# Kernel tuning notes

Measured on AMD Instinct MI355X. Metric: run time of the kernel, lower is better.

## Reference

```python
import jax, jax.numpy as jnp
import numpy as np

DIM = 512
HEADS = 8
DIM_HEAD = 64
INNER = HEADS * DIM_HEAD


def setup_inputs() -> dict:
    key = jax.random.key(0)
    k1, k2, k3, k4 = jax.random.split(key, 4)
    x = jax.random.normal(k1, (4, 8192, DIM), dtype=jnp.float32)
    # nn.Linear(dim, inner*3, bias=False): weight applied as x @ W^T; store transposed form [dim, 3*inner]
    w_qkv = jax.random.normal(k2, (DIM, 3 * INNER), dtype=jnp.float32) / np.sqrt(DIM)
    w_out = jax.random.normal(k3, (INNER, DIM), dtype=jnp.float32) / np.sqrt(INNER)
    b_out = jax.random.normal(k4, (DIM,), dtype=jnp.float32) * 0.01
    return {"x": x, "w_qkv": w_qkv, "w_out": w_out, "b_out": b_out}


def reference(x, w_qkv, w_out, b_out):
    b, n, d = x.shape
    qkv = x @ w_qkv  # [b, n, 3*inner]
    q, k, v = jnp.split(qkv, 3, axis=-1)

    def to_heads(t):
        return t.reshape(b, n, HEADS, DIM_HEAD).transpose(0, 2, 1, 3)  # [b,h,n,dh]

    q, k, v = map(to_heads, (q, k, v))
    q = jax.nn.elu(q) + 1.0
    k = jax.nn.elu(k) + 1.0
    # kv summary: [b,h,dh,dh]
    kv = jnp.einsum('bhnd,bhnm->bhdm', k, v)
    # normalizer z: [b,h,n]  (note: original does NOT apply self.scale)
    z = 1.0 / (jnp.einsum('bhnd,bhd->bhn', q, k.sum(axis=2)) + 1e-6)
    out = jnp.einsum('bhnd,bhdm->bhnm', q, kv) * z[..., None]  # [b,h,n,dh]
    out = out.transpose(0, 2, 1, 3).reshape(b, n, INNER)
    return out @ w_out + b_out
```

## Files before the change

kernel.cpp:

```cpp
#include <hip/hip_runtime.h>
#include <hip/hip_bf16.h>

#define B_SZ 4
#define SEQ 8192
#define DIM 512
#define HEADS 8
#define DH 64
#define INNER 512
#define QKV_COLS 1536
#define M_TOT (B_SZ * SEQ)
#define BHN (B_SZ * HEADS)

typedef __bf16 bf16x8 __attribute__((ext_vector_type(8)));
typedef __bf16 bf16x4 __attribute__((ext_vector_type(4)));
typedef float f32x4 __attribute__((ext_vector_type(4)));

__device__ __forceinline__ float elu1(float x) {
    return x > 0.f ? x + 1.f : __expf(x);
}

__device__ __forceinline__ void gl_lds16(const void* g, void* l) {
    __builtin_amdgcn_global_load_lds(
        (const __attribute__((address_space(1))) unsigned int*)g,
        (__attribute__((address_space(3))) unsigned int*)l, 16, 0, 0);
}

#define MFMA16(a, b, c) __builtin_amdgcn_mfma_f32_16x16x32_bf16(a, b, c, 0, 0, 0)
#define BARRIER() asm volatile("s_barrier" ::: "memory")

__global__ void convert_all(const float* __restrict__ x,
                            const float* __restrict__ w_qkv,
                            const float* __restrict__ w_out,
                            __bf16* __restrict__ xb,
                            __bf16* __restrict__ wqkv_t,
                            __bf16* __restrict__ wout_t) {
    const int NX = M_TOT * DIM / 4;
    int id = blockIdx.x * 256 + threadIdx.x;
    if (id < NX) {
        float4 f = reinterpret_cast<const float4*>(x)[id];
        bf16x4 h = {(__bf16)f.x, (__bf16)f.y, (__bf16)f.z, (__bf16)f.w};
        reinterpret_cast<bf16x4*>(xb)[id] = h;
        return;
    }
    int id2 = id - NX;
    if (id2 < QKV_COLS * DIM) {
        int n = id2 / DIM, k = id2 % DIM;
        wqkv_t[id2] = (__bf16)w_qkv[k * QKV_COLS + n];
    } else {
        int id3 = id2 - QKV_COLS * DIM;
        if (id3 < INNER * DIM) {
            int n = id3 / DIM, k = id3 % DIM;
            wout_t[id3] = (__bf16)w_out[k * DIM + n];
        }
    }
}

#define TSTR 136
__launch_bounds__(256, 2)
__global__ void gemm_qkv(const __bf16* __restrict__ xb,
                         const __bf16* __restrict__ wqkv_t,
                         __bf16* __restrict__ q_ws,
                         __bf16* __restrict__ kT_ws,
                         __bf16* __restrict__ vT_ws) {
    __shared__ __attribute__((aligned(16))) char smem[128 * TSTR * 2];
    __bf16* As = (__bf16*)smem;
    __bf16* Bs = (__bf16*)(smem + 16384);
    __bf16* T  = (__bf16*)smem;

    const int tid = threadIdx.x;
    const int wid = tid >> 6;
    const int lane = tid & 63;
    const int wm = wid >> 1, wn = wid & 1;
    const int lq = lane >> 4, lr = lane & 15;
    const int f  = blockIdx.y * gridDim.x + blockIdx.x;
    const int xc = f & 7, sl = f >> 3;
    const int ml = sl / 12, nn = sl % 12;
    const int m0 = (xc * 32 + ml) * 128;
    const int n0 = nn * 128;
    const int lrow = lane >> 3;
    const int lsw  = ((lane & 7) ^ lrow) * 8;

    f32x4 acc[4][4] = {};

    for (int kb = 0; kb < DIM; kb += 64) {
#pragma unroll
        for (int t = 0; t < 4; ++t) {
            int qi = wid * 4 + t;
            int row = qi * 8 + lrow;
            gl_lds16(&xb[(size_t)(m0 + row) * DIM + kb + lsw], &As[qi * 512]);
            gl_lds16(&wqkv_t[(size_t)(n0 + row) * DIM + kb + lsw], &Bs[qi * 512]);
        }
        __syncthreads();
#pragma unroll
        for (int ks = 0; ks < 2; ++ks) {
            const int csw = ((ks * 4 + lq) ^ (lr & 7)) * 8;
            bf16x8 af[4], bfv[4];
#pragma unroll
            for (int i = 0; i < 4; ++i)
                af[i] = *reinterpret_cast<const bf16x8*>(
                    &As[(wm * 64 + i * 16 + lr) * 64 + csw]);
#pragma unroll
            for (int j = 0; j < 4; ++j)
                bfv[j] = *reinterpret_cast<const bf16x8*>(
                    &Bs[(wn * 64 + j * 16 + lr) * 64 + csw]);
#pragma unroll
            for (int i = 0; i < 4; ++i)
#pragma unroll
                for (int j = 0; j < 4; ++j)
                    acc[i][j] = MFMA16(af[i], bfv[j], acc[i][j]);
        }
        __syncthreads();
    }

    const int which = n0 / INNER;
    const int n0w = n0 % INNER;
    const int b = m0 / SEQ;
    const int nbase = m0 % SEQ;

    if (which == 0) {
#pragma unroll
        for (int i = 0; i < 4; ++i)
#pragma unroll
            for (int j = 0; j < 4; ++j) {
                int col = wn * 64 + j * 16 + lr;
#pragma unroll
                for (int r = 0; r < 4; ++r)
                    T[(wm * 64 + i * 16 + lq * 4 + r) * TSTR + col] =
                        (__bf16)elu1(acc[i][j][r]);
            }
        __syncthreads();
#pragma unroll
        for (int it = 0; it < 8; ++it) {
            int c = tid + it * 256;
            int row = c >> 4, dc = (c & 15) * 8;
            bf16x8 v = *reinterpret_cast<const bf16x8*>(&T[row * TSTR + dc]);
            int col = n0w + dc;
            int h = col >> 6, d = col & 63;
            *reinterpret_cast<bf16x8*>(
                &q_ws[(((size_t)(b * HEADS + h)) * SEQ + nbase + row) * DH + d]) = v;
        }
    } else {
        __bf16* dst = (which == 1) ? kT_ws : vT_ws;
#pragma unroll
        for (int i = 0; i < 4; ++i)
#pragma unroll
            for (int j = 0; j < 4; ++j) {
                int col = wn * 64 + j * 16 + lr;
                int rowb = wm * 64 + i * 16 + lq * 4;
                bf16x4 h4;
#pragma unroll
                for (int r = 0; r < 4; ++r) {
                    float v = acc[i][j][r];
                    h4[r] = (__bf16)((which == 1) ? elu1(v) : v);
                }
                *reinterpret_cast<bf16x4*>(&T[col * TSTR + rowb]) = h4;
            }
        __syncthreads();
#pragma unroll
        for (int it = 0; it < 8; ++it) {
            int c = tid + it * 256;
            int colIdx = c >> 4, rc = (c & 15) * 8;
            bf16x8 v = *reinterpret_cast<const bf16x8*>(&T[colIdx * TSTR + rc]);
            int gcol = n0w + colIdx;
            int h = gcol >> 6, d = gcol & 63;
            *reinterpret_cast<bf16x8*>(
                &dst[(((size_t)(b * HEADS + h)) * DH + d) * SEQ + nbase + rc]) = v;
        }
    }
}

__device__ __forceinline__ void gemm256_core(
    const __bf16* __restrict__ Am, const __bf16* __restrict__ Bm,
    int m0, int n0, char* smem, f32x4 acc[8][4])
{
    const int tid = threadIdx.x;
    const int wid = tid >> 6;
    const int lane = tid & 63;
    const int wm = wid >> 2, wn = wid & 3;
    const int lq = lane >> 4, lr = lane & 15;
    const int lrow = lane >> 3;
    const int lsw  = ((lane & 7) ^ lrow) * 8;

    __bf16* const As0 = (__bf16*)smem;
    __bf16* const Bs0 = (__bf16*)(smem + 32768);
    __bf16* const As1 = (__bf16*)(smem + 65536);
    __bf16* const Bs1 = (__bf16*)(smem + 98304);

    const int csw0 = ((0 + lq) ^ (lr & 7)) * 8;
    const int csw1 = ((4 + lq) ^ (lr & 7)) * 8;

    auto stageB = [&](__bf16* Bs, int kt, int u) {
        gl_lds16(&Bm[(size_t)(n0 + u * 64 + wid * 8 + lrow) * 512 + kt * 64 + lsw],
                 Bs + (u * 64 + wid * 8) * 64);
    };
    auto stageA = [&](__bf16* As, int kt, int s2) {
        int gr = (wid < 4) ? (s2 * 32 + wid * 8) : (128 + s2 * 32 + (wid - 4) * 8);
        gl_lds16(&Am[(size_t)(m0 + gr + lrow) * 512 + kt * 64 + lsw],
                 As + gr * 64);
    };
    auto ldA = [&](const __bf16* As, int m, int csw) -> bf16x8 {
        return *reinterpret_cast<const bf16x8*>(As + (wm * 128 + m * 16 + lr) * 64 + csw);
    };
    auto ldB = [&](const __bf16* Bs, int n, int csw) -> bf16x8 {
        return *reinterpret_cast<const bf16x8*>(Bs + (wn * 64 + n * 16 + lr) * 64 + csw);
    };

    stageB(Bs0, 0, 0); stageB(Bs0, 0, 1); stageB(Bs0, 0, 2); stageB(Bs0, 0, 3);
    stageA(As0, 0, 0); stageA(As0, 0, 1); stageA(As0, 0, 2); stageA(As0, 0, 3);
    asm volatile("s_waitcnt vmcnt(3)" ::: "memory");
    BARRIER();

#pragma unroll 2
    for (int t = 0; t < 8; ++t) {
        __bf16* const As  = (t & 1) ? As1 : As0;
        __bf16* const Bs  = (t & 1) ? Bs1 : Bs0;
        __bf16* const Asn = (t & 1) ? As0 : As1;
        __bf16* const Bsn = (t & 1) ? Bs0 : Bs1;
        const bool pf = (t < 7);
        bf16x8 bfr[4][2];

        {
            bf16x8 a00 = ldA(As, 0, csw0), a01 = ldA(As, 0, csw1);
            bf16x8 a10 = ldA(As, 1, csw0), a11 = ldA(As, 1, csw1);
#pragma unroll
            for (int n = 0; n < 4; ++n) { bfr[n][0] = ldB(Bs, n, csw0); bfr[n][1] = ldB(Bs, n, csw1); }
            if (pf) { stageB(Bsn, t + 1, 0); stageB(Bsn, t + 1, 1); }
            __builtin_amdgcn_s_setprio(1);
#pragma unroll
            for (int n = 0; n < 4; ++n) {
                acc[0][n] = MFMA16(a00, bfr[n][0], acc[0][n]);
                acc[0][n] = MFMA16(a01, bfr[n][1], acc[0][n]);
                acc[1][n] = MFMA16(a10, bfr[n][0], acc[1][n]);
                acc[1][n] = MFMA16(a11, bfr[n][1], acc[1][n]);
            }
            __builtin_amdgcn_s_setprio(0);
            if (pf) asm volatile("s_waitcnt vmcnt(4)" ::: "memory");
            else    asm volatile("s_waitcnt vmcnt(2)" ::: "memory");
            BARRIER();
        }
        {
            bf16x8 a00 = ldA(As, 2, csw0), a01 = ldA(As, 2, csw1);
            bf16x8 a10 = ldA(As, 3, csw0), a11 = ldA(As, 3, csw1);
            if (pf) { stageB(Bsn, t + 1, 2); stageB(Bsn, t + 1, 3); }
            __builtin_amdgcn_s_setprio(1);
#pragma unroll
            for (int n = 0; n < 4; ++n) {
                acc[2][n] = MFMA16(a00, bfr[n][0], acc[2][n]);
                acc[2][n] = MFMA16(a01, bfr[n][1], acc[2][n]);
                acc[3][n] = MFMA16(a10, bfr[n][0], acc[3][n]);
                acc[3][n] = MFMA16(a11, bfr[n][1], acc[3][n]);
            }
            __builtin_amdgcn_s_setprio(0);
            if (pf) asm volatile("s_waitcnt vmcnt(5)" ::: "memory");
            else    asm volatile("s_waitcnt vmcnt(1)" ::: "memory");
            BARRIER();
        }
        {
            bf16x8 a00 = ldA(As, 4, csw0), a01 = ldA(As, 4, csw1);
            bf16x8 a10 = ldA(As, 5, csw0), a11 = ldA(As, 5, csw1);
            if (pf) { stageA(Asn, t + 1, 0); stageA(Asn, t + 1, 1); }
            __builtin_amdgcn_s_setprio(1);
#pragma unroll
            for (int n = 0; n < 4; ++n) {
                acc[4][n] = MFMA16(a00, bfr[n][0], acc[4][n]);
                acc[4][n] = MFMA16(a01, bfr[n][1], acc[4][n]);
                acc[5][n] = MFMA16(a10, bfr[n][0], acc[5][n]);
                acc[5][n] = MFMA16(a11, bfr[n][1], acc[5][n]);
            }
            __builtin_amdgcn_s_setprio(0);
            if (pf) asm volatile("s_waitcnt vmcnt(6)" ::: "memory");
            else    asm volatile("s_waitcnt vmcnt(0)" ::: "memory");
            BARRIER();
        }
        {
            bf16x8 a00 = ldA(As, 6, csw0), a01 = ldA(As, 6, csw1);
            bf16x8 a10 = ldA(As, 7, csw0), a11 = ldA(As, 7, csw1);
            if (pf) { stageA(Asn, t + 1, 2); stageA(Asn, t + 1, 3); }
            __builtin_amdgcn_s_setprio(1);
#pragma unroll
            for (int n = 0; n < 4; ++n) {
                acc[6][n] = MFMA16(a00, bfr[n][0], acc[6][n]);
                acc[6][n] = MFMA16(a01, bfr[n][1], acc[6][n]);
                acc[7][n] = MFMA16(a10, bfr[n][0], acc[7][n]);
                acc[7][n] = MFMA16(a11, bfr[n][1], acc[7][n]);
            }
            __builtin_amdgcn_s_setprio(0);
            if (pf) asm volatile("s_waitcnt vmcnt(3)" ::: "memory");
            BARRIER();
        }
    }
}

__launch_bounds__(256, 2)
__global__ void kv_reduce(const __bf16* __restrict__ kT,
                          const __bf16* __restrict__ vT,
                          float* __restrict__ kv_t,
                          float* __restrict__ ksum) {
    __shared__ __attribute__((aligned(16))) __bf16 Ks[64][136];
    __shared__ __attribute__((aligned(16))) __bf16 Vs[64][136];
    const int tid = threadIdx.x;
    const int wid = tid >> 6;
    const int lane = tid & 63;
    const int lq = lane >> 4, lr = lane & 15;
    const int bh = blockIdx.y;
    const int n0 = blockIdx.x * 512;
    const size_t base = (size_t)bh * DH * SEQ;
    f32x4 acc[4] = {};
    f32x4 acc1 = {};
    bf16x8 ones8;
#pragma unroll
    for (int e = 0; e < 8; ++e) ones8[e] = (__bf16)1.f;

    for (int ch = 0; ch < 4; ++ch) {
        int nc = n0 + ch * 128;
#pragma unroll
        for (int t = 0; t < 4; ++t) {
            int c = tid + t * 256;
            int row = c >> 4, kc = (c & 15) * 8;
            *reinterpret_cast<bf16x8*>(&Ks[row][kc]) =
                *reinterpret_cast<const bf16x8*>(&kT[base + (size_t)row * SEQ + nc + kc]);
            *reinterpret_cast<bf16x8*>(&Vs[row][kc]) =
                *reinterpret_cast<const bf16x8*>(&vT[base + (size_t)row * SEQ + nc + kc]);
        }
        __syncthreads();
#pragma unroll
        for (int ks = 0; ks < 4; ++ks) {
            bf16x8 a = *reinterpret_cast<const bf16x8*>(&Ks[wid * 16 + lr][ks * 32 + lq * 8]);
            acc1 = MFMA16(a, ones8, acc1);
#pragma unroll
            for (int j = 0; j < 4; ++j) {
                bf16x8 b = *reinterpret_cast<const bf16x8*>(&Vs[j * 16 + lr][ks * 32 + lq * 8]);
                acc[j] = MFMA16(a, b, acc[j]);
            }
        }
        __syncthreads();
    }
    float* dst = kv_t + (size_t)bh * DH * DH;
#pragma unroll
    for (int j = 0; j < 4; ++j) {
        int m = j * 16 + lr;
#pragma unroll
        for (int r = 0; r < 4; ++r) {
            int d = wid * 16 + lq * 4 + r;
            atomicAdd(&dst[m * DH + d], acc[j][r]);
        }
    }
    if (lr == 0) {
#pragma unroll
        for (int r = 0; r < 4; ++r)
            atomicAdd(&ksum[bh * DH + wid * 16 + lq * 4 + r], acc1[r]);
    }
}

__launch_bounds__(256, 2)
__global__ void attn_kernel(const __bf16* __restrict__ q_ws,
                            const float* __restrict__ kv_t,
                            const float* __restrict__ ksum,
                            __bf16* __restrict__ attn) {
    __shared__ __attribute__((aligned(16))) __bf16 Qs[128][72];
    __shared__ __attribute__((aligned(16))) __bf16 KVs[64][72];
    __shared__ float zs[128];
    __shared__ float ks_s[64];
    const int tid = threadIdx.x;
    const int wid = tid >> 6, lane = tid & 63;
    const int lq = lane >> 4, lr = lane & 15;
    const int bh = blockIdx.y;
    const int b = bh >> 3, h = bh & 7;
    const int n0 = blockIdx.x * 128;
    const size_t qbase = ((size_t)bh * SEQ + n0) * DH;

#pragma unroll
    for (int t = 0; t < 4; ++t) {
        int c = tid + t * 256;
        int row = c >> 3, kc = (c & 7) * 8;
        *reinterpret_cast<bf16x8*>(&Qs[row][kc]) =
            *reinterpret_cast<const bf16x8*>(&q_ws[qbase + (size_t)row * DH + kc]);
    }
    const float* kvsrc = kv_t + (size_t)bh * DH * DH;
#pragma unroll
    for (int t = 0; t < 4; ++t) {
        int c = tid + t * 256;
        int m = c >> 4, dc = (c & 15) * 4;
        float4 f = *reinterpret_cast<const float4*>(&kvsrc[m * DH + dc]);
        bf16x4 h4 = {(__bf16)f.x, (__bf16)f.y, (__bf16)f.z, (__bf16)f.w};
        *reinterpret_cast<bf16x4*>(&KVs[m][dc]) = h4;
    }
    if (tid < 64) ks_s[tid] = ksum[bh * DH + tid];
    __syncthreads();
    {
        int row = tid >> 1, part = tid & 1;
        float s = 0.f;
#pragma unroll
        for (int j = 0; j < 32; ++j)
            s += (float)Qs[row][part * 32 + j] * ks_s[part * 32 + j];
        s += __shfl_xor(s, 1, 64);
        if (part == 0) zs[row] = 1.f / (s + 1e-6f);
    }
    __syncthreads();

    f32x4 acc[2][4] = {};
#pragma unroll
    for (int ks = 0; ks < 2; ++ks) {
        bf16x8 a0 = *reinterpret_cast<const bf16x8*>(&Qs[wid * 32 + lr][ks * 32 + lq * 8]);
        bf16x8 a1 = *reinterpret_cast<const bf16x8*>(&Qs[wid * 32 + 16 + lr][ks * 32 + lq * 8]);
#pragma unroll
        for (int j = 0; j < 4; ++j) {
            bf16x8 bfr = *reinterpret_cast<const bf16x8*>(&KVs[j * 16 + lr][ks * 32 + lq * 8]);
            acc[0][j] = MFMA16(a0, bfr, acc[0][j]);
            acc[1][j] = MFMA16(a1, bfr, acc[1][j]);
        }
    }
    __syncthreads();
#pragma unroll
    for (int mt = 0; mt < 2; ++mt)
#pragma unroll
        for (int j = 0; j < 4; ++j) {
            int m = j * 16 + lr;
#pragma unroll
            for (int r = 0; r < 4; ++r) {
                int row = wid * 32 + mt * 16 + lq * 4 + r;
                Qs[row][m] = (__bf16)(acc[mt][j][r] * zs[row]);
            }
        }
    __syncthreads();
#pragma unroll
    for (int it = 0; it < 4; ++it) {
        int c = tid + it * 256;
        int row = c >> 3, mc = (c & 7) * 8;
        bf16x8 v = *reinterpret_cast<const bf16x8*>(&Qs[row][mc]);
        *reinterpret_cast<bf16x8*>(
            &attn[((size_t)(b * SEQ + n0 + row)) * INNER + h * DH + mc]) = v;
    }
}

__launch_bounds__(512, 2)
__global__ void gemm_out(const __bf16* __restrict__ attn,
                         const __bf16* __restrict__ wout_t,
                         const float* __restrict__ b_out,
                         float* __restrict__ out) {
    __shared__ __attribute__((aligned(16))) char smem[131072];
    const int f  = blockIdx.y * gridDim.x + blockIdx.x;
    const int xc = f & 7, sl = f >> 3;
    const int m0 = (xc * 16 + (sl >> 1)) * 256;
    const int n0 = (sl & 1) * 256;

    f32x4 acc[8][4] = {};
    gemm256_core(attn, wout_t, m0, n0, smem, acc);

    const int tid = threadIdx.x;
    const int wid = tid >> 6;
    const int lane = tid & 63;
    const int wm = wid >> 2, wn = wid & 3;
    const int lq = lane >> 4, lr = lane & 15;

#pragma unroll
    for (int n = 0; n < 4; ++n) {
        int col = n0 + wn * 64 + n * 16 + lr;
        float bias = b_out[col];
#pragma unroll
        for (int m = 0; m < 8; ++m) {
            int row = m0 + wm * 128 + m * 16 + lq * 4;
#pragma unroll
            for (int r = 0; r < 4; ++r)
                out[(size_t)(row + r) * DIM + col] = acc[m][n][r] + bias;
        }
    }
}

extern "C" void kernel_launch(void* const* d_in, const int* in_sizes, int n_in,
                              void* d_out, int out_size, void* d_ws, size_t ws_size,
                              hipStream_t stream) {
    (void)in_sizes; (void)n_in; (void)out_size; (void)ws_size;
    const float* x     = (const float*)d_in[0];
    const float* w_qkv = (const float*)d_in[1];
    const float* w_out = (const float*)d_in[2];
    const float* b_out = (const float*)d_in[3];
    float* out = (float*)d_out;

    char* ws = (char*)d_ws;
    size_t off = 0;
    auto alloc = [&](size_t bytes) {
        char* p = ws + off;
        off += (bytes + 255) & ~(size_t)255;
        return p;
    };
    __bf16* xb     = (__bf16*)alloc((size_t)M_TOT * DIM * 2);
    __bf16* attn   = xb;
    __bf16* q_ws   = (__bf16*)alloc((size_t)BHN * SEQ * DH * 2);
    __bf16* kT_ws  = (__bf16*)alloc((size_t)BHN * SEQ * DH * 2);
    __bf16* vT_ws  = (__bf16*)alloc((size_t)BHN * SEQ * DH * 2);
    float*  kv_t   = (float*)alloc((size_t)BHN * DH * DH * 4 + (size_t)BHN * DH * 4);
    float*  ksum   = kv_t + (size_t)BHN * DH * DH;
    __bf16* wqkv_t = (__bf16*)alloc((size_t)QKV_COLS * DIM * 2);
    __bf16* wout_t = (__bf16*)alloc((size_t)INNER * DIM * 2);

    hipMemsetAsync(kv_t, 0, (size_t)BHN * DH * DH * 4 + (size_t)BHN * DH * 4, stream);
    convert_all<<<dim3(M_TOT * DIM / 4 / 256 + (QKV_COLS * DIM + INNER * DIM) / 256),
                  256, 0, stream>>>(x, w_qkv, w_out, xb, wqkv_t, wout_t);
    gemm_qkv<<<dim3(M_TOT / 128, QKV_COLS / 128), 256, 0, stream>>>(
        xb, wqkv_t, q_ws, kT_ws, vT_ws);
    kv_reduce<<<dim3(16, BHN), 256, 0, stream>>>(kT_ws, vT_ws, kv_t, ksum);
    attn_kernel<<<dim3(SEQ / 128, BHN), 256, 0, stream>>>(q_ws, kv_t, ksum, attn);
    gemm_out<<<dim3(M_TOT / 256, DIM / 256), 512, 0, stream>>>(attn, wout_t, b_out, out);
}
```

Measured before the change: 267.9 us.

## Tile weight transpose through LDS, double-buffer kv_reduce loads, vectorize z dot

The weight transpose-convert now goes through a padded 32x33 shared-memory tile, so both the global reads and writes are coalesced instead of strided. kv_reduce gains double-buffered LDS and register prefetch, so the next chunk's global loads overlap the current chunk's MFMAs. The z normalizer in attn_kernel reads Q with 8-wide vector LDS loads. These changes add shared memory and register use, and the weight conversion is only a small part of total time.

```diff
diff --git a/kernel.cpp b/kernel.cpp
--- a/kernel.cpp
+++ b/kernel.cpp
@@ -28,30 +28,46 @@
 #define MFMA16(a, b, c) __builtin_amdgcn_mfma_f32_16x16x32_bf16(a, b, c, 0, 0, 0)
 #define BARRIER() asm volatile("s_barrier" ::: "memory")
 
+#define XBLKS 16384
 __global__ void convert_all(const float* __restrict__ x,
                             const float* __restrict__ w_qkv,
                             const float* __restrict__ w_out,
                             __bf16* __restrict__ xb,
                             __bf16* __restrict__ wqkv_t,
                             __bf16* __restrict__ wout_t) {
-    const int NX = M_TOT * DIM / 4;
-    int id = blockIdx.x * 256 + threadIdx.x;
-    if (id < NX) {
+    const int tid = threadIdx.x;
+    const int bid = blockIdx.x;
+    if (bid < XBLKS) {
+        int id = bid * 256 + tid;
         float4 f = reinterpret_cast<const float4*>(x)[id];
         bf16x4 h = {(__bf16)f.x, (__bf16)f.y, (__bf16)f.z, (__bf16)f.w};
         reinterpret_cast<bf16x4*>(xb)[id] = h;
         return;
     }
-    int id2 = id - NX;
-    if (id2 < QKV_COLS * DIM) {
-        int n = id2 / DIM, k = id2 % DIM;
-        wqkv_t[id2] = (__bf16)w_qkv[k * QKV_COLS + n];
+    __shared__ float tile[32][33];
+    int tb = bid - XBLKS;
+    const float* src; __bf16* dst; int k0, n0, scols;
+    if (tb < 768) {
+        int kt = tb & 15, nt = tb >> 4;
+        k0 = kt * 32; n0 = nt * 32; src = w_qkv; dst = wqkv_t; scols = QKV_COLS;
     } else {
-        int id3 = id2 - QKV_COLS * DIM;
-        if (id3 < INNER * DIM) {
-            int n = id3 / DIM, k = id3 % DIM;
-            wout_t[id3] = (__bf16)w_out[k * DIM + n];
-        }
+        tb -= 768;
+        int kt = tb & 15, nt = tb >> 4;
+        k0 = kt * 32; n0 = nt * 32; src = w_out; dst = wout_t; scols = DIM;
+    }
+    {
+        int c = tid & 31, r = tid >> 5;
+#pragma unroll
+        for (int p = 0; p < 4; ++p)
+            tile[r + p * 8][c] = src[(size_t)(k0 + r + p * 8) * scols + n0 + c];
+    }
+    __syncthreads();
+    {
+        int k = tid & 31, n = tid >> 5;
+#pragma unroll
+        for (int p = 0; p < 4; ++p)
+            dst[(size_t)(n0 + n + p * 8) * DIM + k0 + k] =
+                (__bf16)tile[k][n + p * 8];
     }
 }
 
@@ -296,8 +312,8 @@
                           const __bf16* __restrict__ vT,
                           float* __restrict__ kv_t,
                           float* __restrict__ ksum) {
-    __shared__ __attribute__((aligned(16))) __bf16 Ks[64][136];
-    __shared__ __attribute__((aligned(16))) __bf16 Vs[64][136];
+    __shared__ __attribute__((aligned(16))) __bf16 Ks[2][64][136];
+    __shared__ __attribute__((aligned(16))) __bf16 Vs[2][64][136];
     const int tid = threadIdx.x;
     const int wid = tid >> 6;
     const int lane = tid & 63;
@@ -311,28 +327,42 @@
 #pragma unroll
     for (int e = 0; e < 8; ++e) ones8[e] = (__bf16)1.f;
 
+    const int srow = tid >> 4, skc = (tid & 15) * 8;
+    bf16x8 kr[4], vr[4];
+    auto load_regs = [&](int ch) {
+        int nc = n0 + ch * 128;
+#pragma unroll
+        for (int t = 0; t < 4; ++t) {
+            int row = srow + t * 16;
+            kr[t] = *reinterpret_cast<const bf16x8*>(&kT[base + (size_t)row * SEQ + nc + skc]);
+            vr[t] = *reinterpret_cast<const bf16x8*>(&vT[base + (size_t)row * SEQ + nc + skc]);
+        }
+    };
+    auto st_lds = [&](int buf) {
+#pragma unroll
+        for (int t = 0; t < 4; ++t) {
+            int row = srow + t * 16;
+            *reinterpret_cast<bf16x8*>(&Ks[buf][row][skc]) = kr[t];
+            *reinterpret_cast<bf16x8*>(&Vs[buf][row][skc]) = vr[t];
+        }
+    };
+
+    load_regs(0); st_lds(0);
+    __syncthreads();
     for (int ch = 0; ch < 4; ++ch) {
-        int nc = n0 + ch * 128;
-#pragma unroll
-        for (int t = 0; t < 4; ++t) {
-            int c = tid + t * 256;
-            int row = c >> 4, kc = (c & 15) * 8;
-            *reinterpret_cast<bf16x8*>(&Ks[row][kc]) =
-                *reinterpret_cast<const bf16x8*>(&kT[base + (size_t)row * SEQ + nc + kc]);
-            *reinterpret_cast<bf16x8*>(&Vs[row][kc]) =
-                *reinterpret_cast<const bf16x8*>(&vT[base + (size_t)row * SEQ + nc + kc]);
-        }
-        __syncthreads();
+        const int buf = ch & 1;
+        if (ch < 3) load_regs(ch + 1);
 #pragma unroll
         for (int ks = 0; ks < 4; ++ks) {
-            bf16x8 a = *reinterpret_cast<const bf16x8*>(&Ks[wid * 16 + lr][ks * 32 + lq * 8]);
+            bf16x8 a = *reinterpret_cast<const bf16x8*>(&Ks[buf][wid * 16 + lr][ks * 32 + lq * 8]);
             acc1 = MFMA16(a, ones8, acc1);
 #pragma unroll
             for (int j = 0; j < 4; ++j) {
-                bf16x8 b = *reinterpret_cast<const bf16x8*>(&Vs[j * 16 + lr][ks * 32 + lq * 8]);
+                bf16x8 b = *reinterpret_cast<const bf16x8*>(&Vs[buf][j * 16 + lr][ks * 32 + lq * 8]);
                 acc[j] = MFMA16(a, b, acc[j]);
             }
         }
+        if (ch < 3) st_lds(buf ^ 1);
         __syncthreads();
     }
     float* dst = kv_t + (size_t)bh * DH * DH;
@@ -391,8 +421,12 @@
         int row = tid >> 1, part = tid & 1;
         float s = 0.f;
 #pragma unroll
-        for (int j = 0; j < 32; ++j)
-            s += (float)Qs[row][part * 32 + j] * ks_s[part * 32 + j];
+        for (int c = 0; c < 4; ++c) {
+            bf16x8 v = *reinterpret_cast<const bf16x8*>(&Qs[row][part * 32 + c * 8]);
+            const float* kp = &ks_s[part * 32 + c * 8];
+#pragma unroll
+            for (int j = 0; j < 8; ++j) s += (float)v[j] * kp[j];
+        }
         s += __shfl_xor(s, 1, 64);
         if (part == 0) zs[row] = 1.f / (s + 1e-6f);
     }
@@ -495,8 +529,8 @@
     __bf16* wout_t = (__bf16*)alloc((size_t)INNER * DIM * 2);
 
     hipMemsetAsync(kv_t, 0, (size_t)BHN * DH * DH * 4 + (size_t)BHN * DH * 4, stream);
-    convert_all<<<dim3(M_TOT * DIM / 4 / 256 + (QKV_COLS * DIM + INNER * DIM) / 256),
-                  256, 0, stream>>>(x, w_qkv, w_out, xb, wqkv_t, wout_t);
+    convert_all<<<dim3(XBLKS + 768 + 256), 256, 0, stream>>>(
+        x, w_qkv, w_out, xb, wqkv_t, wout_t);
     gemm_qkv<<<dim3(M_TOT / 128, QKV_COLS / 128), 256, 0, stream>>>(
         xb, wqkv_t, q_ws, kT_ws, vT_ws);
     kv_reduce<<<dim3(16, BHN), 256, 0, stream>>>(kT_ws, vT_ws, kv_t, ksum);
```

Result: no change. 264.3 us (-1.3%).
